# Performance work log

Measured on AMD Instinct MI355X. Metric: run time of the kernel, lower is better.

Reference implementation:

```python
import jax, jax.numpy as jnp
import numpy as np

N, E, D = 100000, 1600000, 64
BN_EPS = 1e-5
ATT_SLOPE = 0.2   # GATConv attention leaky relu slope
ACT_SLOPE = 0.01  # nn.LeakyReLU default


def setup_inputs() -> dict:
    key = jax.random.key(0)
    ks = jax.random.split(key, 12)
    s = 1.0 / np.sqrt(D)
    return {
        "x": jax.random.normal(ks[0], (N, D), jnp.float32),
        "W1": jax.random.normal(ks[1], (D, D), jnp.float32) * s,
        "att_src1": jax.random.normal(ks[2], (D,), jnp.float32) * s,
        "att_dst1": jax.random.normal(ks[3], (D,), jnp.float32) * s,
        "bias1": jnp.zeros((D,), jnp.float32),
        "bn_gamma": jnp.ones((D,), jnp.float32),
        "bn_beta": jnp.zeros((D,), jnp.float32),
        "W2": jax.random.normal(ks[4], (D, D), jnp.float32) * s,
        "att_src2": jax.random.normal(ks[5], (D,), jnp.float32) * s,
        "att_dst2": jax.random.normal(ks[6], (D,), jnp.float32) * s,
        "bias2": jnp.zeros((D,), jnp.float32),
        "edge_index": jax.random.randint(ks[7], (2, E), 0, N, jnp.int64 if jax.config.jax_enable_x64 else jnp.int32),
    }


def gat_conv(x, src, dst, W, a_src, a_dst, bias):
    # h: [N, D] transformed features
    h = x @ W
    # per-edge attention logits (gather of per-node scores)
    logit = jax.nn.leaky_relu((h @ a_src)[src] + (h @ a_dst)[dst], ATT_SLOPE)
    # segment softmax over incoming edges of each destination node
    m = jax.ops.segment_max(logit, dst, num_segments=N)
    e = jnp.exp(logit - m[dst])
    z = jax.ops.segment_sum(e, dst, num_segments=N)
    alpha = e / z[dst]                              # [E']
    msg = h[src] * alpha[:, None]                   # [E', D] gather + weight
    return jax.ops.segment_sum(msg, dst, num_segments=N) + bias


def reference(x, W1, att_src1, att_dst1, bias1, bn_gamma, bn_beta,
              W2, att_src2, att_dst2, bias2, edge_index):
    # PyG GATConv adds self-loops by default
    loops = jnp.arange(N, dtype=edge_index.dtype)
    src = jnp.concatenate([edge_index[0], loops])
    dst = jnp.concatenate([edge_index[1], loops])

    x0 = x
    h = gat_conv(x, src, dst, W1, att_src1, att_dst1, bias1)
    # BatchNorm1d in training mode: batch stats, biased variance
    mu = h.mean(axis=0)
    var = h.var(axis=0)
    h = (h - mu) * jax.lax.rsqrt(var + BN_EPS) * bn_gamma + bn_beta
    h = jax.nn.leaky_relu(h, ACT_SLOPE)
    # dropout p=0.0 -> no-op
    out = gat_conv(h, src, dst, W2, att_src2, att_dst2, bias2)
    # mean over stacked [input x, final node_emb]
    return 0.5 * (x0 + out)
```

## Files before the change

kernel.cpp:

```cpp
#include <hip/hip_runtime.h>
#include <math.h>

#define D 64
#define CAP 64
#define NBB 128
#define NPB 256

__device__ __forceinline__ float lrelu(float x, float s) { return x > 0.f ? x : s * x; }

__device__ __forceinline__ unsigned f2bf(float f) {
    unsigned b = __builtin_bit_cast(unsigned, f);
    return (b + 0x7fffu + ((b >> 16) & 1u)) >> 16;
}
__device__ __forceinline__ float bflo(unsigned u) { return __builtin_bit_cast(float, u << 16); }
__device__ __forceinline__ float bfhi(unsigned u) { return __builtin_bit_cast(float, u & 0xffff0000u); }

__device__ __forceinline__ void mm_rows(const float* __restrict__ xin,
        const float* __restrict__ W, const float* __restrict__ a_src, const float* __restrict__ a_dst,
        const float* __restrict__ bn_sum, const float* __restrict__ bn_sumsq,
        const float* __restrict__ gamma, const float* __restrict__ beta, int apply_bn,
        unsigned* __restrict__ hb, float* __restrict__ ssrc, float* __restrict__ sdst,
        int N, int worker, int nworkers, int lane, int wv) {
    float w[D];
    #pragma unroll
    for (int k = 0; k < D; ++k) w[k] = W[k * D + lane];
    float asv = a_src[lane], adv = a_dst[lane];
    float sc = 1.f, sh = 0.f;
    if (apply_bn) {
        float mu = bn_sum[lane] / (float)N;
        float var = bn_sumsq[lane] / (float)N - mu * mu;
        float rs = rsqrtf(var + 1e-5f);
        sc = rs * gamma[lane];
        sh = beta[lane] - mu * sc;
    }
    for (int r = worker * 4 + wv; r < N; r += nworkers * 4) {
        float v = xin[(size_t)r * D + lane];
        if (apply_bn) { v = v * sc + sh; v = v > 0.f ? v : 0.01f * v; }
        int vi = __builtin_bit_cast(int, v);
        float a0 = 0.f, a1 = 0.f, a2 = 0.f, a3 = 0.f;
        #pragma unroll
        for (int k = 0; k < D; k += 4) {
            float b0 = __builtin_bit_cast(float, __builtin_amdgcn_readlane(vi, k + 0));
            float b1 = __builtin_bit_cast(float, __builtin_amdgcn_readlane(vi, k + 1));
            float b2 = __builtin_bit_cast(float, __builtin_amdgcn_readlane(vi, k + 2));
            float b3 = __builtin_bit_cast(float, __builtin_amdgcn_readlane(vi, k + 3));
            a0 = fmaf(b0, w[k + 0], a0);
            a1 = fmaf(b1, w[k + 1], a1);
            a2 = fmaf(b2, w[k + 2], a2);
            a3 = fmaf(b3, w[k + 3], a3);
        }
        float acc = (a0 + a1) + (a2 + a3);
        float accp = __shfl_xor(acc, 1, 64);
        unsigned packed = f2bf(acc) | (f2bf(accp) << 16);
        if (!(lane & 1)) hb[(size_t)r * 32 + (lane >> 1)] = packed;
        float v1 = acc * asv, v2 = acc * adv;
        #pragma unroll
        for (int off = 32; off; off >>= 1) {
            v1 += __shfl_xor(v1, off, 64);
            v2 += __shfl_xor(v2, off, 64);
        }
        if (lane == 0) { ssrc[r] = v1; sdst[r] = v2; }
    }
}

__global__ __launch_bounds__(256) void k_bin_mm1(const int* __restrict__ ei, int E,
        int* __restrict__ bin_ptr, unsigned* __restrict__ binned, int BCAP,
        const float* __restrict__ xin, const float* __restrict__ W,
        const float* __restrict__ a_src, const float* __restrict__ a_dst,
        unsigned* __restrict__ hb, float* __restrict__ ssrc, float* __restrict__ sdst, int N) {
    __shared__ int hist[512], cur[512];
    int tid = threadIdx.x, lane = tid & 63, wv = tid >> 6;
    if (blockIdx.x < NBB) {
        int nb = (N + NPB - 1) >> 8;
        for (int t = tid; t < nb; t += 256) hist[t] = 0;
        __syncthreads();
        int nq4 = E >> 2;
        int qpb = (nq4 + NBB - 1) / NBB;
        int q0 = blockIdx.x * qpb;
        int q1 = q0 + qpb; if (q1 > nq4) q1 = nq4;
        const int4* s4 = (const int4*)ei;
        const int4* d4 = (const int4*)(ei + E);
        for (int i = q0 + tid; i < q1; i += 256) {
            int4 d = d4[i];
            atomicAdd(&hist[d.x >> 8], 1);
            atomicAdd(&hist[d.y >> 8], 1);
            atomicAdd(&hist[d.z >> 8], 1);
            atomicAdd(&hist[d.w >> 8], 1);
        }
        if (blockIdx.x == 0 && tid < (E & 3)) {
            int dd = ei[E + (nq4 << 2) + tid];
            atomicAdd(&hist[dd >> 8], 1);
        }
        __syncthreads();
        for (int t = tid; t < nb; t += 256)
            cur[t] = hist[t] ? atomicAdd(&bin_ptr[t], hist[t]) : 0;
        __syncthreads();
        for (int i = q0 + tid; i < q1; i += 256) {
            int4 s = s4[i];
            int4 d = d4[i];
            int t0 = d.x >> 8, t1 = d.y >> 8, t2 = d.z >> 8, t3 = d.w >> 8;
            int p0 = atomicAdd(&cur[t0], 1);
            int p1 = atomicAdd(&cur[t1], 1);
            int p2 = atomicAdd(&cur[t2], 1);
            int p3 = atomicAdd(&cur[t3], 1);
            if (p0 < BCAP) binned[(size_t)t0 * BCAP + p0] = (unsigned)s.x | ((unsigned)(d.x & 255) << 17);
            if (p1 < BCAP) binned[(size_t)t1 * BCAP + p1] = (unsigned)s.y | ((unsigned)(d.y & 255) << 17);
            if (p2 < BCAP) binned[(size_t)t2 * BCAP + p2] = (unsigned)s.z | ((unsigned)(d.z & 255) << 17);
            if (p3 < BCAP) binned[(size_t)t3 * BCAP + p3] = (unsigned)s.w | ((unsigned)(d.w & 255) << 17);
        }
        if (blockIdx.x == 0 && tid < (E & 3)) {
            int i = (nq4 << 2) + tid;
            int ss = ei[i], dd = ei[E + i];
            int t = dd >> 8;
            int p = atomicAdd(&cur[t], 1);
            if (p < BCAP) binned[(size_t)t * BCAP + p] = (unsigned)ss | ((unsigned)(dd & 255) << 17);
        }
    } else {
        mm_rows(xin, W, a_src, a_dst, nullptr, nullptr, nullptr, nullptr, 0,
                hb, ssrc, sdst, N, blockIdx.x - NBB, gridDim.x - NBB, lane, wv);
    }
}

__global__ __launch_bounds__(256) void k_scatter(const unsigned* __restrict__ binned,
        const int* __restrict__ bin_ptr, int BCAP,
        int* __restrict__ col, int* __restrict__ cnt, int N) {
    __shared__ int cur[NPB];
    int tid = threadIdx.x;
    int b = blockIdx.x;
    cur[tid] = 0;
    __syncthreads();
    int cntb = bin_ptr[b]; if (cntb > BCAP) cntb = BCAP;
    const unsigned* base = binned + (size_t)b * BCAP;
    for (int i = tid; i < cntb; i += 256) {
        unsigned e = base[i];
        int dl = (int)(e >> 17);
        int k = atomicAdd(&cur[dl], 1);
        if (k < CAP) col[((size_t)((b << 8) + dl) << 6) + k] = (int)(e & 0x1FFFFu);
    }
    __syncthreads();
    int node = (b << 8) + tid;
    if (node < N) cnt[node] = cur[tid];
}

__global__ __launch_bounds__(256) void k_mm_att(const float* __restrict__ xin,
        const float* __restrict__ W, const float* __restrict__ a_src, const float* __restrict__ a_dst,
        const float* __restrict__ bn_sum, const float* __restrict__ bn_sumsq,
        const float* __restrict__ gamma, const float* __restrict__ beta,
        unsigned* __restrict__ hb, float* __restrict__ ssrc, float* __restrict__ sdst, int N) {
    int tid = threadIdx.x, lane = tid & 63, wv = tid >> 6;
    mm_rows(xin, W, a_src, a_dst, bn_sum, bn_sumsq, gamma, beta, 1,
            hb, ssrc, sdst, N, blockIdx.x, gridDim.x, lane, wv);
}

#define AGG_ISSUE(P, q) { \
    int sA_ = __shfl(sal0.x, (q), 16), sB_ = __shfl(sal0.y, (q), 16); \
    int sC_ = __shfl(sal0.z, (q), 16), sD_ = __shfl(sal0.w, (q), 16); \
    P##A = h2[(size_t)sA_ * 16 + sl]; P##B = h2[(size_t)sB_ * 16 + sl]; \
    P##C = h2[(size_t)sC_ * 16 + sl]; P##D = h2[(size_t)sD_ * 16 + sl]; }

#define AGG_CONSUME(P, i) { \
    float eA_ = __shfl(e0, (i), 16), eB_ = __shfl(e1, (i), 16); \
    float eC_ = __shfl(e2, (i), 16), eD_ = __shfl(e3, (i), 16); \
    acc.x = fmaf(eA_, bflo(P##A.x), acc.x); acc.y = fmaf(eA_, bfhi(P##A.x), acc.y); \
    acc.z = fmaf(eA_, bflo(P##A.y), acc.z); acc.w = fmaf(eA_, bfhi(P##A.y), acc.w); \
    acc.x = fmaf(eB_, bflo(P##B.x), acc.x); acc.y = fmaf(eB_, bfhi(P##B.x), acc.y); \
    acc.z = fmaf(eB_, bflo(P##B.y), acc.z); acc.w = fmaf(eB_, bfhi(P##B.y), acc.w); \
    acc.x = fmaf(eC_, bflo(P##C.x), acc.x); acc.y = fmaf(eC_, bfhi(P##C.x), acc.y); \
    acc.z = fmaf(eC_, bflo(P##C.y), acc.z); acc.w = fmaf(eC_, bfhi(P##C.y), acc.w); \
    acc.x = fmaf(eD_, bflo(P##D.x), acc.x); acc.y = fmaf(eD_, bfhi(P##D.x), acc.y); \
    acc.z = fmaf(eD_, bflo(P##D.y), acc.z); acc.w = fmaf(eD_, bfhi(P##D.y), acc.w); }

__global__ __launch_bounds__(256) void k_csr_agg(const int* __restrict__ col,
        const int* __restrict__ cnt,
        const float* __restrict__ ssrc, const float* __restrict__ sdst,
        const unsigned* __restrict__ hb, const float* __restrict__ bias,
        const float* __restrict__ x, float* __restrict__ out,
        float* __restrict__ bn_sum, float* __restrict__ bn_sumsq, int mode, int N) {
    __shared__ float sbn1[D], sbn2[D];
    int tid = threadIdx.x;
    int lane = tid & 63;
    int sl = lane & 15;
    if (mode == 0) {
        if (tid < D) { sbn1[tid] = 0.f; sbn2[tid] = 0.f; }
        __syncthreads();
    }
    int sgid = (blockIdx.x * 256 + tid) >> 4;
    int stride = gridDim.x * 16;
    const uint2* h2 = (const uint2*)hb;
    float4 s1 = make_float4(0, 0, 0, 0), s2 = make_float4(0, 0, 0, 0);

    auto loadA = [&](int node, int& dg, int4& sal, float& ssn, float& sdn) {
        int nn = (node < N) ? node : sgid;
        int dgl = cnt[nn]; dgl = dgl > CAP ? CAP : dgl;
        int4 c = ((const int4*)(col + ((size_t)nn << 6)))[sl];
        int eb = sl << 2;
        sal.x = (eb + 0 < dgl) ? c.x : nn;
        sal.y = (eb + 1 < dgl) ? c.y : nn;
        sal.z = (eb + 2 < dgl) ? c.z : nn;
        sal.w = (eb + 3 < dgl) ? c.w : nn;
        dg = dgl; ssn = ssrc[nn]; sdn = sdst[nn];
    };

    if (sgid < N) {
        int dg0, dg1; int4 sal0, sal1;
        float ssn0, sdn0, ssn1, sdn1;
        float4 g0;
        loadA(sgid,          dg0, sal0, ssn0, sdn0);
        loadA(sgid + stride, dg1, sal1, ssn1, sdn1);
        g0.x = ssrc[sal0.x]; g0.y = ssrc[sal0.y];
        g0.z = ssrc[sal0.z]; g0.w = ssrc[sal0.w];

        for (int n = sgid; n < N; n += stride) {
            uint2 hv = h2[(size_t)n * 16 + sl];
            int Q = dg0 > 0 ? ((dg0 + 3) >> 2) : 1;
            uint2 p0A, p0B, p0C, p0D, p1A, p1B, p1C, p1D, p2A, p2B, p2C, p2D;
            AGG_ISSUE(p0, 0)
            if (Q > 1) AGG_ISSUE(p1, 1)
            if (Q > 2) AGG_ISSUE(p2, 2)

            int dg2; int4 sal2; float ssn2, sdn2;
            loadA(n + 2 * stride, dg2, sal2, ssn2, sdn2);

            float4 g1;
            g1.x = ssrc[sal1.x]; g1.y = ssrc[sal1.y];
            g1.z = ssrc[sal1.z]; g1.w = ssrc[sal1.w];

            int eb = sl << 2;
            float e0 = (eb + 0 < dg0) ? __expf(lrelu(g0.x + sdn0, 0.2f)) : 0.f;
            float e1 = (eb + 1 < dg0) ? __expf(lrelu(g0.y + sdn0, 0.2f)) : 0.f;
            float e2 = (eb + 2 < dg0) ? __expf(lrelu(g0.z + sdn0, 0.2f)) : 0.f;
            float e3 = (eb + 3 < dg0) ? __expf(lrelu(g0.w + sdn0, 0.2f)) : 0.f;
            float z = (e0 + e1) + (e2 + e3);
            #pragma unroll
            for (int off = 1; off <= 8; off <<= 1) z += __shfl_xor(z, off, 64);
            float es = __expf(lrelu(ssn0 + sdn0, 0.2f));
            z += es;
            float4 acc;
            acc.x = es * bflo(hv.x); acc.y = es * bfhi(hv.x);
            acc.z = es * bflo(hv.y); acc.w = es * bfhi(hv.y);

            int i = 0;
            while (true) {
                AGG_CONSUME(p0, i)
                if (i + 3 < Q) AGG_ISSUE(p0, i + 3)
                if (++i >= Q) break;
                AGG_CONSUME(p1, i)
                if (i + 3 < Q) AGG_ISSUE(p1, i + 3)
                if (++i >= Q) break;
                AGG_CONSUME(p2, i)
                if (i + 3 < Q) AGG_ISSUE(p2, i + 3)
                if (++i >= Q) break;
            }

            float inv = 1.f / z;
            float4 b4 = ((const float4*)bias)[sl];
            float4 v;
            v.x = acc.x * inv + b4.x; v.y = acc.y * inv + b4.y;
            v.z = acc.z * inv + b4.z; v.w = acc.w * inv + b4.w;
            if (mode == 0) {
                ((float4*)out)[(size_t)n * 16 + sl] = v;
                s1.x += v.x; s1.y += v.y; s1.z += v.z; s1.w += v.w;
                s2.x += v.x * v.x; s2.y += v.y * v.y;
                s2.z += v.z * v.z; s2.w += v.w * v.w;
            } else {
                float4 xv = ((const float4*)x)[(size_t)n * 16 + sl];
                v.x = 0.5f * (xv.x + v.x); v.y = 0.5f * (xv.y + v.y);
                v.z = 0.5f * (xv.z + v.z); v.w = 0.5f * (xv.w + v.w);
                ((float4*)out)[(size_t)n * 16 + sl] = v;
            }
            dg0 = dg1; sal0 = sal1; ssn0 = ssn1; sdn0 = sdn1; g0 = g1;
            dg1 = dg2; sal1 = sal2; ssn1 = ssn2; sdn1 = sdn2;
        }
    }
    if (mode == 0) {
        int c = sl * 4;
        atomicAdd(&sbn1[c + 0], s1.x); atomicAdd(&sbn1[c + 1], s1.y);
        atomicAdd(&sbn1[c + 2], s1.z); atomicAdd(&sbn1[c + 3], s1.w);
        atomicAdd(&sbn2[c + 0], s2.x); atomicAdd(&sbn2[c + 1], s2.y);
        atomicAdd(&sbn2[c + 2], s2.z); atomicAdd(&sbn2[c + 3], s2.w);
        __syncthreads();
        if (tid < D) {
            atomicAdd(&bn_sum[tid], sbn1[tid]);
            atomicAdd(&bn_sumsq[tid], sbn2[tid]);
        }
    }
}

extern "C" void kernel_launch(void* const* d_in, const int* in_sizes, int n_in,
                              void* d_out, int out_size, void* d_ws, size_t ws_size,
                              hipStream_t stream) {
    const float* x     = (const float*)d_in[0];
    const float* W1    = (const float*)d_in[1];
    const float* as1   = (const float*)d_in[2];
    const float* ad1   = (const float*)d_in[3];
    const float* b1    = (const float*)d_in[4];
    const float* gamma = (const float*)d_in[5];
    const float* beta  = (const float*)d_in[6];
    const float* W2    = (const float*)d_in[7];
    const float* as2   = (const float*)d_in[8];
    const float* ad2   = (const float*)d_in[9];
    const float* b2    = (const float*)d_in[10];
    const int*   ei    = (const int*)d_in[11];
    int N = in_sizes[0] / D;
    int E = in_sizes[11] / 2;
    float* out = (float*)d_out;

    float* ws = (float*)d_ws;
    unsigned* hb = (unsigned*)ws;
    float* ssrc = (float*)(hb + (size_t)N * 32);
    float* sdst = ssrc + N;
    int* cnt    = (int*)(sdst + N);
    int* binp   = cnt + N;
    float* bn   = (float*)(binp + 512);
    int* colarr = (int*)(bn + 128);

    int nb = (N + NPB - 1) >> 8;
    int BCAP = E / nb + (E / nb) / 4 + 256;
    if ((size_t)nb * BCAP > (size_t)out_size) BCAP = (int)((size_t)out_size / (size_t)nb);
    unsigned* binned = (unsigned*)d_out;

    dim3 blk(256);

    hipMemsetAsync(binp, 0, 512 * 4 + 512, stream);

    k_bin_mm1<<<2048, blk, 0, stream>>>(ei, E, binp, binned, BCAP,
                                        x, W1, as1, ad1, hb, ssrc, sdst, N);

    k_scatter<<<nb, blk, 0, stream>>>(binned, binp, BCAP, colarr, cnt, N);

    k_csr_agg<<<2048, blk, 0, stream>>>(colarr, cnt, ssrc, sdst, hb, b1,
                                        nullptr, out, bn, bn + 64, 0, N);

    k_mm_att<<<2048, blk, 0, stream>>>(out, W2, as2, ad2, bn, bn + 64, gamma, beta,
                                       hb, ssrc, sdst, N);
    k_csr_agg<<<2048, blk, 0, stream>>>(colarr, cnt, ssrc, sdst, hb, b2,
                                        x, out, bn, bn + 64, 1, N);
}
```

Measured before the change: 298.9 us.

## Fuse CSR scatter into aggregation via per-block LDS adjacency from 64-node bins

Shrinks destination bins from 256 to 64 nodes and removes the separate scatter kernel. Each aggregation block now rebuilds its 64 nodes' adjacency lists in shared memory from the binned edge list, and reads that list for both GAT layers. This drops the global col/cnt arrays and their write and read traffic, plus one launch. In exchange each layer redoes the LDS bucketing, the grid is fixed at about 1563 blocks of 16-lane groups handling 4 nodes each, and the 16KB of shared memory per block may cut occupancy.

Result: faster. 286.1 us (-4.3%).

```diff
diff --git a/kernel.cpp b/kernel.cpp
--- a/kernel.cpp
+++ b/kernel.cpp
@@ -4,7 +4,8 @@
 #define D 64
 #define CAP 64
 #define NBB 128
-#define NPB 256
+#define NPB 64
+#define NBINMAX 2048
 
 __device__ __forceinline__ float lrelu(float x, float s) { return x > 0.f ? x : s * x; }
 
@@ -68,10 +69,10 @@
         const float* __restrict__ xin, const float* __restrict__ W,
         const float* __restrict__ a_src, const float* __restrict__ a_dst,
         unsigned* __restrict__ hb, float* __restrict__ ssrc, float* __restrict__ sdst, int N) {
-    __shared__ int hist[512], cur[512];
+    __shared__ int hist[NBINMAX], cur[NBINMAX];
     int tid = threadIdx.x, lane = tid & 63, wv = tid >> 6;
     if (blockIdx.x < NBB) {
-        int nb = (N + NPB - 1) >> 8;
+        int nb = (N + NPB - 1) >> 6;
         for (int t = tid; t < nb; t += 256) hist[t] = 0;
         __syncthreads();
         int nq4 = E >> 2;
@@ -82,14 +83,14 @@
         const int4* d4 = (const int4*)(ei + E);
         for (int i = q0 + tid; i < q1; i += 256) {
             int4 d = d4[i];
-            atomicAdd(&hist[d.x >> 8], 1);
-            atomicAdd(&hist[d.y >> 8], 1);
-            atomicAdd(&hist[d.z >> 8], 1);
-            atomicAdd(&hist[d.w >> 8], 1);
+            atomicAdd(&hist[d.x >> 6], 1);
+            atomicAdd(&hist[d.y >> 6], 1);
+            atomicAdd(&hist[d.z >> 6], 1);
+            atomicAdd(&hist[d.w >> 6], 1);
         }
         if (blockIdx.x == 0 && tid < (E & 3)) {
             int dd = ei[E + (nq4 << 2) + tid];
-            atomicAdd(&hist[dd >> 8], 1);
+            atomicAdd(&hist[dd >> 6], 1);
         }
         __syncthreads();
         for (int t = tid; t < nb; t += 256)
@@ -98,48 +99,27 @@
         for (int i = q0 + tid; i < q1; i += 256) {
             int4 s = s4[i];
             int4 d = d4[i];
-            int t0 = d.x >> 8, t1 = d.y >> 8, t2 = d.z >> 8, t3 = d.w >> 8;
+            int t0 = d.x >> 6, t1 = d.y >> 6, t2 = d.z >> 6, t3 = d.w >> 6;
             int p0 = atomicAdd(&cur[t0], 1);
             int p1 = atomicAdd(&cur[t1], 1);
             int p2 = atomicAdd(&cur[t2], 1);
             int p3 = atomicAdd(&cur[t3], 1);
-            if (p0 < BCAP) binned[(size_t)t0 * BCAP + p0] = (unsigned)s.x | ((unsigned)(d.x & 255) << 17);
-            if (p1 < BCAP) binned[(size_t)t1 * BCAP + p1] = (unsigned)s.y | ((unsigned)(d.y & 255) << 17);
-            if (p2 < BCAP) binned[(size_t)t2 * BCAP + p2] = (unsigned)s.z | ((unsigned)(d.z & 255) << 17);
-            if (p3 < BCAP) binned[(size_t)t3 * BCAP + p3] = (unsigned)s.w | ((unsigned)(d.w & 255) << 17);
+            if (p0 < BCAP) binned[(size_t)t0 * BCAP + p0] = (unsigned)s.x | ((unsigned)(d.x & 63) << 17);
+            if (p1 < BCAP) binned[(size_t)t1 * BCAP + p1] = (unsigned)s.y | ((unsigned)(d.y & 63) << 17);
+            if (p2 < BCAP) binned[(size_t)t2 * BCAP + p2] = (unsigned)s.z | ((unsigned)(d.z & 63) << 17);
+            if (p3 < BCAP) binned[(size_t)t3 * BCAP + p3] = (unsigned)s.w | ((unsigned)(d.w & 63) << 17);
         }
         if (blockIdx.x == 0 && tid < (E & 3)) {
             int i = (nq4 << 2) + tid;
             int ss = ei[i], dd = ei[E + i];
-            int t = dd >> 8;
+            int t = dd >> 6;
             int p = atomicAdd(&cur[t], 1);
-            if (p < BCAP) binned[(size_t)t * BCAP + p] = (unsigned)ss | ((unsigned)(dd & 255) << 17);
+            if (p < BCAP) binned[(size_t)t * BCAP + p] = (unsigned)ss | ((unsigned)(dd & 63) << 17);
         }
     } else {
         mm_rows(xin, W, a_src, a_dst, nullptr, nullptr, nullptr, nullptr, 0,
                 hb, ssrc, sdst, N, blockIdx.x - NBB, gridDim.x - NBB, lane, wv);
     }
-}
-
-__global__ __launch_bounds__(256) void k_scatter(const unsigned* __restrict__ binned,
-        const int* __restrict__ bin_ptr, int BCAP,
-        int* __restrict__ col, int* __restrict__ cnt, int N) {
-    __shared__ int cur[NPB];
-    int tid = threadIdx.x;
-    int b = blockIdx.x;
-    cur[tid] = 0;
-    __syncthreads();
-    int cntb = bin_ptr[b]; if (cntb > BCAP) cntb = BCAP;
-    const unsigned* base = binned + (size_t)b * BCAP;
-    for (int i = tid; i < cntb; i += 256) {
-        unsigned e = base[i];
-        int dl = (int)(e >> 17);
-        int k = atomicAdd(&cur[dl], 1);
-        if (k < CAP) col[((size_t)((b << 8) + dl) << 6) + k] = (int)(e & 0x1FFFFu);
-    }
-    __syncthreads();
-    int node = (b << 8) + tid;
-    if (node < N) cnt[node] = cur[tid];
 }
 
 __global__ __launch_bounds__(256) void k_mm_att(const float* __restrict__ xin,
@@ -170,107 +150,132 @@
     acc.x = fmaf(eD_, bflo(P##D.x), acc.x); acc.y = fmaf(eD_, bfhi(P##D.x), acc.y); \
     acc.z = fmaf(eD_, bflo(P##D.y), acc.z); acc.w = fmaf(eD_, bfhi(P##D.y), acc.w); }
 
-__global__ __launch_bounds__(256) void k_csr_agg(const int* __restrict__ col,
-        const int* __restrict__ cnt,
+__global__ __launch_bounds__(256) void k_agg(const unsigned* __restrict__ binned,
+        const int* __restrict__ bin_ptr, int BCAP,
         const float* __restrict__ ssrc, const float* __restrict__ sdst,
         const unsigned* __restrict__ hb, const float* __restrict__ bias,
         const float* __restrict__ x, float* __restrict__ out,
         float* __restrict__ bn_sum, float* __restrict__ bn_sumsq, int mode, int N) {
+    __shared__ int colL[NPB][CAP];
+    __shared__ int cntL[NPB];
+    __shared__ float ssL[NPB], sdL[NPB];
     __shared__ float sbn1[D], sbn2[D];
     int tid = threadIdx.x;
-    int lane = tid & 63;
-    int sl = lane & 15;
-    if (mode == 0) {
-        if (tid < D) { sbn1[tid] = 0.f; sbn2[tid] = 0.f; }
-        __syncthreads();
-    }
-    int sgid = (blockIdx.x * 256 + tid) >> 4;
-    int stride = gridDim.x * 16;
+    int sl = tid & 15;
+    int g = tid >> 4;
+    int b = blockIdx.x;
+    int n0 = b << 6;
+
+    if (tid < NPB) {
+        cntL[tid] = 0;
+        int nd = n0 + tid;
+        ssL[tid] = (nd < N) ? ssrc[nd] : 0.f;
+        sdL[tid] = (nd < N) ? sdst[nd] : 0.f;
+    }
+    if (mode == 0 && tid < D) { sbn1[tid] = 0.f; sbn2[tid] = 0.f; }
+    __syncthreads();
+
+    int m = bin_ptr[b]; if (m > BCAP) m = BCAP;
+    {
+        const unsigned* base = binned + (size_t)b * BCAP;
+        for (int i = tid; i < m; i += 256) {
+            unsigned e = base[i];
+            int dl = (int)(e >> 17);
+            int k = atomicAdd(&cntL[dl], 1);
+            if (k < CAP) colL[dl][k] = (int)(e & 0x1FFFFu);
+        }
+    }
+    __syncthreads();
+
     const uint2* h2 = (const uint2*)hb;
     float4 s1 = make_float4(0, 0, 0, 0), s2 = make_float4(0, 0, 0, 0);
 
-    auto loadA = [&](int node, int& dg, int4& sal, float& ssn, float& sdn) {
-        int nn = (node < N) ? node : sgid;
-        int dgl = cnt[nn]; dgl = dgl > CAP ? CAP : dgl;
-        int4 c = ((const int4*)(col + ((size_t)nn << 6)))[sl];
+    auto loadSal = [&](int d, int& dg, int4& sal) {
+        int dgl = cntL[d]; if (dgl > CAP) dgl = CAP;
+        int4 c = ((const int4*)colL[d])[sl];
         int eb = sl << 2;
-        sal.x = (eb + 0 < dgl) ? c.x : nn;
-        sal.y = (eb + 1 < dgl) ? c.y : nn;
-        sal.z = (eb + 2 < dgl) ? c.z : nn;
-        sal.w = (eb + 3 < dgl) ? c.w : nn;
-        dg = dgl; ssn = ssrc[nn]; sdn = sdst[nn];
+        int nd = n0 + d;
+        int self = (nd < N) ? nd : 0;
+        sal.x = (eb + 0 < dgl) ? c.x : self;
+        sal.y = (eb + 1 < dgl) ? c.y : self;
+        sal.z = (eb + 2 < dgl) ? c.z : self;
+        sal.w = (eb + 3 < dgl) ? c.w : self;
+        dg = dgl;
     };
 
-    if (sgid < N) {
-        int dg0, dg1; int4 sal0, sal1;
-        float ssn0, sdn0, ssn1, sdn1;
-        float4 g0;
-        loadA(sgid,          dg0, sal0, ssn0, sdn0);
-        loadA(sgid + stride, dg1, sal1, ssn1, sdn1);
-        g0.x = ssrc[sal0.x]; g0.y = ssrc[sal0.y];
-        g0.z = ssrc[sal0.z]; g0.w = ssrc[sal0.w];
-
-        for (int n = sgid; n < N; n += stride) {
-            uint2 hv = h2[(size_t)n * 16 + sl];
-            int Q = dg0 > 0 ? ((dg0 + 3) >> 2) : 1;
-            uint2 p0A, p0B, p0C, p0D, p1A, p1B, p1C, p1D, p2A, p2B, p2C, p2D;
-            AGG_ISSUE(p0, 0)
-            if (Q > 1) AGG_ISSUE(p1, 1)
-            if (Q > 2) AGG_ISSUE(p2, 2)
-
-            int dg2; int4 sal2; float ssn2, sdn2;
-            loadA(n + 2 * stride, dg2, sal2, ssn2, sdn2);
-
-            float4 g1;
+    int dg0; int4 sal0;
+    loadSal(g, dg0, sal0);
+    float4 g0;
+    g0.x = ssrc[sal0.x]; g0.y = ssrc[sal0.y];
+    g0.z = ssrc[sal0.z]; g0.w = ssrc[sal0.w];
+
+    #pragma unroll
+    for (int idx = 0; idx < 4; ++idx) {
+        int d = g + (idx << 4);
+        int nd = n0 + d;
+        int ndc = (nd < N) ? nd : 0;
+        uint2 hv = h2[(size_t)ndc * 16 + sl];
+        int Q = dg0 > 0 ? ((dg0 + 3) >> 2) : 1;
+        uint2 p0A, p0B, p0C, p0D, p1A, p1B, p1C, p1D, p2A, p2B, p2C, p2D;
+        AGG_ISSUE(p0, 0)
+        if (Q > 1) AGG_ISSUE(p1, 1)
+        if (Q > 2) AGG_ISSUE(p2, 2)
+
+        int dg1 = 0; int4 sal1 = make_int4(0, 0, 0, 0);
+        float4 g1 = make_float4(0, 0, 0, 0);
+        if (idx < 3) {
+            loadSal(d + 16, dg1, sal1);
             g1.x = ssrc[sal1.x]; g1.y = ssrc[sal1.y];
             g1.z = ssrc[sal1.z]; g1.w = ssrc[sal1.w];
-
-            int eb = sl << 2;
-            float e0 = (eb + 0 < dg0) ? __expf(lrelu(g0.x + sdn0, 0.2f)) : 0.f;
-            float e1 = (eb + 1 < dg0) ? __expf(lrelu(g0.y + sdn0, 0.2f)) : 0.f;
-            float e2 = (eb + 2 < dg0) ? __expf(lrelu(g0.z + sdn0, 0.2f)) : 0.f;
-            float e3 = (eb + 3 < dg0) ? __expf(lrelu(g0.w + sdn0, 0.2f)) : 0.f;
-            float z = (e0 + e1) + (e2 + e3);
-            #pragma unroll
-            for (int off = 1; off <= 8; off <<= 1) z += __shfl_xor(z, off, 64);
-            float es = __expf(lrelu(ssn0 + sdn0, 0.2f));
-            z += es;
-            float4 acc;
-            acc.x = es * bflo(hv.x); acc.y = es * bfhi(hv.x);
-            acc.z = es * bflo(hv.y); acc.w = es * bfhi(hv.y);
-
-            int i = 0;
-            while (true) {
-                AGG_CONSUME(p0, i)
-                if (i + 3 < Q) AGG_ISSUE(p0, i + 3)
-                if (++i >= Q) break;
-                AGG_CONSUME(p1, i)
-                if (i + 3 < Q) AGG_ISSUE(p1, i + 3)
-                if (++i >= Q) break;
-                AGG_CONSUME(p2, i)
-                if (i + 3 < Q) AGG_ISSUE(p2, i + 3)
-                if (++i >= Q) break;
-            }
-
+        }
+
+        float sdn = sdL[d];
+        int eb = sl << 2;
+        float e0 = (eb + 0 < dg0) ? __expf(lrelu(g0.x + sdn, 0.2f)) : 0.f;
+        float e1 = (eb + 1 < dg0) ? __expf(lrelu(g0.y + sdn, 0.2f)) : 0.f;
+        float e2 = (eb + 2 < dg0) ? __expf(lrelu(g0.z + sdn, 0.2f)) : 0.f;
+        float e3 = (eb + 3 < dg0) ? __expf(lrelu(g0.w + sdn, 0.2f)) : 0.f;
+        float z = (e0 + e1) + (e2 + e3);
+        #pragma unroll
+        for (int off = 1; off <= 8; off <<= 1) z += __shfl_xor(z, off, 64);
+        float es = __expf(lrelu(ssL[d] + sdn, 0.2f));
+        z += es;
+        float4 acc;
+        acc.x = es * bflo(hv.x); acc.y = es * bfhi(hv.x);
+        acc.z = es * bflo(hv.y); acc.w = es * bfhi(hv.y);
+
+        int i = 0;
+        while (true) {
+            AGG_CONSUME(p0, i)
+            if (i + 3 < Q) AGG_ISSUE(p0, i + 3)
+            if (++i >= Q) break;
+            AGG_CONSUME(p1, i)
+            if (i + 3 < Q) AGG_ISSUE(p1, i + 3)
+            if (++i >= Q) break;
+            AGG_CONSUME(p2, i)
+            if (i + 3 < Q) AGG_ISSUE(p2, i + 3)
+            if (++i >= Q) break;
+        }
+
+        if (nd < N) {
             float inv = 1.f / z;
             float4 b4 = ((const float4*)bias)[sl];
             float4 v;
             v.x = acc.x * inv + b4.x; v.y = acc.y * inv + b4.y;
             v.z = acc.z * inv + b4.z; v.w = acc.w * inv + b4.w;
             if (mode == 0) {
-                ((float4*)out)[(size_t)n * 16 + sl] = v;
+                ((float4*)out)[(size_t)nd * 16 + sl] = v;
                 s1.x += v.x; s1.y += v.y; s1.z += v.z; s1.w += v.w;
                 s2.x += v.x * v.x; s2.y += v.y * v.y;
                 s2.z += v.z * v.z; s2.w += v.w * v.w;
             } else {
-                float4 xv = ((const float4*)x)[(size_t)n * 16 + sl];
+                float4 xv = ((const float4*)x)[(size_t)nd * 16 + sl];
                 v.x = 0.5f * (xv.x + v.x); v.y = 0.5f * (xv.y + v.y);
                 v.z = 0.5f * (xv.z + v.z); v.w = 0.5f * (xv.w + v.w);
-                ((float4*)out)[(size_t)n * 16 + sl] = v;
+                ((float4*)out)[(size_t)nd * 16 + sl] = v;
             }
-            dg0 = dg1; sal0 = sal1; ssn0 = ssn1; sdn0 = sdn1; g0 = g1;
-            dg1 = dg2; sal1 = sal2; ssn1 = ssn2; sdn1 = sdn2;
-        }
+        }
+        dg0 = dg1; sal0 = sal1; g0 = g1;
     }
     if (mode == 0) {
         int c = sl * 4;
@@ -309,30 +314,25 @@
     unsigned* hb = (unsigned*)ws;
     float* ssrc = (float*)(hb + (size_t)N * 32);
     float* sdst = ssrc + N;
-    int* cnt    = (int*)(sdst + N);
-    int* binp   = cnt + N;
-    float* bn   = (float*)(binp + 512);
-    int* colarr = (int*)(bn + 128);
-
-    int nb = (N + NPB - 1) >> 8;
+    int* binp   = (int*)(sdst + N);
+    float* bn   = (float*)(binp + NBINMAX);
+    unsigned* binned = (unsigned*)(bn + 128);
+
+    int nb = (N + NPB - 1) >> 6;
     int BCAP = E / nb + (E / nb) / 4 + 256;
-    if ((size_t)nb * BCAP > (size_t)out_size) BCAP = (int)((size_t)out_size / (size_t)nb);
-    unsigned* binned = (unsigned*)d_out;
 
     dim3 blk(256);
 
-    hipMemsetAsync(binp, 0, 512 * 4 + 512, stream);
+    hipMemsetAsync(binp, 0, NBINMAX * 4 + 512, stream);
 
     k_bin_mm1<<<2048, blk, 0, stream>>>(ei, E, binp, binned, BCAP,
                                         x, W1, as1, ad1, hb, ssrc, sdst, N);
 
-    k_scatter<<<nb, blk, 0, stream>>>(binned, binp, BCAP, colarr, cnt, N);
-
-    k_csr_agg<<<2048, blk, 0, stream>>>(colarr, cnt, ssrc, sdst, hb, b1,
-                                        nullptr, out, bn, bn + 64, 0, N);
+    k_agg<<<nb, blk, 0, stream>>>(binned, binp, BCAP, ssrc, sdst, hb, b1,
+                                  nullptr, out, bn, bn + 64, 0, N);
 
     k_mm_att<<<2048, blk, 0, stream>>>(out, W2, as2, ad2, bn, bn + 64, gamma, beta,
                                        hb, ssrc, sdst, N);
-    k_csr_agg<<<2048, blk, 0, stream>>>(colarr, cnt, ssrc, sdst, hb, b2,
-                                        x, out, bn, bn + 64, 1, N);
-}
+    k_agg<<<nb, blk, 0, stream>>>(binned, binp, BCAP, ssrc, sdst, hb, b2,
+                                  x, out, bn, bn + 64, 1, N);
+}
```
